# Optimization experiments

Hardware: AMD Instinct MI355X
Metric: run time of the kernel (lower is better)

Reference implementation:

```python
import jax, jax.numpy as jnp
import numpy as np

B, NP, NS = 64, 32, 72
H, F = 4, 64
HD = H * F            # 256
CS, CE = 7, 16
L = 4
NC = 110
EPS = 1e-6


def setup_inputs() -> dict:
    key = jax.random.key(0)
    ks = jax.random.split(key, 32)
    def n(k, shape, s=0.05):
        return (jax.random.normal(k, shape, jnp.float32) * s)
    spatial_obs = jax.random.normal(ks[0], (B, NP, NS), jnp.float32)
    card_context = jax.random.normal(ks[1], (B, CS, CE), jnp.float32)
    adj = (jax.random.uniform(ks[2], (NS, NS)) > 0.85).astype(jnp.float32)
    adj = jnp.maximum(adj, jnp.eye(NS, dtype=jnp.float32))  # self-loops
    return {
        'spatial_obs': spatial_obs,
        'card_context': card_context,
        'adj': adj,
        'ctx_W': n(ks[3], (CS * CE, HD)), 'ctx_b': jnp.zeros((HD,)),
        'lnc_s': jnp.ones((HD,)), 'lnc_b': jnp.zeros((HD,)),
        'in_W': n(ks[4], (NP, HD)), 'in_b': jnp.zeros((HD,)),
        'lnp_s': jnp.ones((L, HD)), 'lnp_b': jnp.zeros((L, HD)),
        'cp_W': n(ks[5], (L, HD, HD)), 'cp_b': jnp.zeros((L, HD)),
        'Wl': n(ks[6], (L, HD, HD)), 'Wr': n(ks[7], (L, HD, HD)),
        'Wa': n(ks[8], (L, H, F)),
        'op_W': n(ks[9], (L, HD, HD)), 'op_b': jnp.zeros((L, HD)),
        'card_W': n(ks[10], (HD, NC)), 'card_b': jnp.zeros((NC,)),
        'at_W': n(ks[11], (HD, 3)), 'at_b': jnp.zeros((3,)),
        'src_W': n(ks[12], (HD, NS)), 'src_b': jnp.zeros((NS,)),
        'tgt_W': n(ks[13], (HD, NS)), 'tgt_b': jnp.zeros((NS,)),
        'v1_W': n(ks[14], (HD, 128)), 'v1_b': jnp.zeros((128,)),
        'v2_W': n(ks[15], (128, 1)), 'v2_b': jnp.zeros((1,)),
    }


def _layernorm(x, s, b):
    m = jnp.mean(x, axis=-1, keepdims=True)
    v = jnp.var(x, axis=-1, keepdims=True)
    return (x - m) * jax.lax.rsqrt(v + EPS) * s + b


def _gatv2(h, adj, Wl, Wr, Wa):
    # h: (B, N, HD); GATv2: e_ij = Wa . LeakyReLU(Wl h_i + Wr h_j)
    b, n, _ = h.shape
    hl = jnp.einsum('bnd,de->bne', h, Wl).reshape(b, n, H, F)
    hr = jnp.einsum('bnd,de->bne', h, Wr).reshape(b, n, H, F)
    e = jax.nn.leaky_relu(hl[:, :, None, :, :] + hr[:, None, :, :, :], 0.2)  # (B,N,N,H,F)
    scores = jnp.einsum('bijhf,hf->bijh', e, Wa)
    scores = jnp.where(adj[None, :, :, None] > 0, scores, -1e9)
    attn = jax.nn.softmax(scores, axis=2)  # softmax over neighbors j
    out = jnp.einsum('bijh,bjhf->bihf', attn, hr)
    return out.reshape(b, n, HD)


def reference(spatial_obs, card_context, adj,
              ctx_W, ctx_b, lnc_s, lnc_b, in_W, in_b,
              lnp_s, lnp_b, cp_W, cp_b, Wl, Wr, Wa, op_W, op_b,
              card_W, card_b, at_W, at_b, src_W, src_b, tgt_W, tgt_b,
              v1_W, v1_b, v2_W, v2_b):
    b = spatial_obs.shape[0]
    ctx = card_context.reshape(b, CS * CE)
    g = jax.nn.relu(_layernorm(ctx @ ctx_W + ctx_b, lnc_s, lnc_b))  # (B, HD)
    x = jnp.einsum('bps,pd->bsd', spatial_obs, in_W) + in_b          # (B, NS, HD)
    for l in range(L):
        h = _layernorm(x, lnp_s[l], lnp_b[l])
        h = h + (g @ cp_W[l] + cp_b[l])[:, None, :]
        hg = _gatv2(h, adj, Wl[l], Wr[l], Wa[l])
        x = x + (hg @ op_W[l] + op_b[l])
    ge = jnp.mean(x, axis=1)  # (B, HD)
    card_logits = ge @ card_W + card_b
    action_type_logits = ge @ at_W + at_b
    src_logits = ge @ src_W + src_b
    tgt_logits = ge @ tgt_W + tgt_b
    value = jnp.tanh(jax.nn.relu(ge @ v1_W + v1_b) @ v2_W + v2_b)
    return (card_logits, action_type_logits, src_logits, tgt_logits, value)
```

## Files before the change

### kernel.cpp

```cpp
#include <hip/hip_runtime.h>
#include <hip/hip_bf16.h>
#include <math.h>

#define B 64
#define NP 32
#define NS 72
#define NH 4
#define NF 64
#define HD 256
#define CTXD 112
#define NL 4
#define NC 110
#define LN_EPS 1e-6f
#define GROWS 8

#define SH 68
#define SA 76

typedef __hip_bfloat16 bf16;

__device__ __forceinline__ float ldv(const float* p, int i) { return p[i]; }
__device__ __forceinline__ float ldv(const bf16* p, int i) { return __bfloat162float(p[i]); }
__device__ __forceinline__ void stv(float* p, int i, float v) { p[i] = v; }
__device__ __forceinline__ void stv(bf16* p, int i, float v) { p[i] = __float2bfloat16(v); }

__global__ void k_detect(const void* adj, int* flag) {
  if (threadIdx.x == 0 && blockIdx.x == 0) {
    *flag = (((const unsigned short*)adj)[0] == 0x3F80u) ? 1 : 0;
  }
}

__device__ __forceinline__ void block_reduce_2(float& a, float& b, float* sred, int t) {
  #pragma unroll
  for (int o = 32; o > 0; o >>= 1) { a += __shfl_down(a, o); b += __shfl_down(b, o); }
  if ((t & 63) == 0) { sred[(t >> 6) * 2] = a; sred[(t >> 6) * 2 + 1] = b; }
  __syncthreads();
  a = sred[0] + sred[2] + sred[4] + sred[6];
  b = sred[1] + sred[3] + sred[5] + sred[7];
}

template <typename T>
__device__ void ctx_body(const T* cardctx, const T* ctxW, const T* ctxb,
                         const T* lncs, const T* lncb, float* g,
                         float* sred, float* sctx) {
  int b = blockIdx.x, t = threadIdx.x;
  if (t < CTXD) sctx[t] = ldv(cardctx, b * CTXD + t);
  __syncthreads();
  float acc = ldv(ctxb, t);
  for (int k = 0; k < CTXD; ++k) acc += sctx[k] * ldv(ctxW, k * HD + t);
  float a = acc, bb = acc * acc;
  block_reduce_2(a, bb, sred, t);
  float mean = a * (1.f / HD);
  float var = bb * (1.f / HD) - mean * mean;
  float r = rsqrtf(var + LN_EPS);
  float v = (acc - mean) * r * ldv(lncs, t) + ldv(lncb, t);
  g[b * HD + t] = fmaxf(v, 0.f);
}
__global__ void __launch_bounds__(256) k_ctx(const void* cardctx, const void* ctxW, const void* ctxb,
                      const void* lncs, const void* lncb, float* g, const int* flag) {
  __shared__ float sred[8];
  __shared__ float sctx[CTXD];
  if (*flag) ctx_body<bf16>((const bf16*)cardctx, (const bf16*)ctxW, (const bf16*)ctxb,
                            (const bf16*)lncs, (const bf16*)lncb, g, sred, sctx);
  else ctx_body<float>((const float*)cardctx, (const float*)ctxW, (const float*)ctxb,
                       (const float*)lncs, (const float*)lncb, g, sred, sctx);
}

template <typename T>
__device__ void inproj_body(const T* spat, const T* inW, const T* inb, float* x, float* ssp) {
  int blk = blockIdx.x; int b = blk / NS; int s = blk % NS; int t = threadIdx.x;
  if (t < NP) ssp[t] = ldv(spat, (b * NP + t) * NS + s);
  __syncthreads();
  float acc = ldv(inb, t);
  #pragma unroll 8
  for (int p = 0; p < NP; ++p) acc += ssp[p] * ldv(inW, p * HD + t);
  x[blk * HD + t] = acc;
}
__global__ void __launch_bounds__(256) k_inproj(const void* spat, const void* inW, const void* inb,
                         float* x, const int* flag) {
  __shared__ float ssp[NP];
  if (*flag) inproj_body<bf16>((const bf16*)spat, (const bf16*)inW, (const bf16*)inb, x, ssp);
  else inproj_body<float>((const float*)spat, (const float*)inW, (const float*)inb, x, ssp);
}

template <typename T>
__device__ void cproj_body(const float* g, const T* cpW, const T* cpb, float* c, int l, float* sg) {
  int b = blockIdx.x, t = threadIdx.x;
  sg[t] = g[b * HD + t];
  __syncthreads();
  const T* W = cpW + l * HD * HD;
  float acc = ldv(cpb, l * HD + t);
  for (int k = 0; k < HD; ++k) acc += sg[k] * ldv(W, k * HD + t);
  c[b * HD + t] = acc;
}
__global__ void __launch_bounds__(256) k_cproj(const float* g, const void* cpW, const void* cpb,
                        float* c, int l, const int* flag) {
  __shared__ float sg[HD];
  if (*flag) cproj_body<bf16>(g, (const bf16*)cpW, (const bf16*)cpb, c, l, sg);
  else cproj_body<float>(g, (const float*)cpW, (const float*)cpb, c, l, sg);
}

template <typename T>
__device__ void lnadd_body(const float* x, const float* c, const T* lnps, const T* lnpb,
                           float* h, int l, float* sred) {
  int row = blockIdx.x, t = threadIdx.x;
  float v = x[row * HD + t];
  float a = v, bb = v * v;
  block_reduce_2(a, bb, sred, t);
  float mean = a * (1.f / HD);
  float var = bb * (1.f / HD) - mean * mean;
  float r = rsqrtf(var + LN_EPS);
  float o = (v - mean) * r * ldv(lnps, l * HD + t) + ldv(lnpb, l * HD + t)
          + c[(row / NS) * HD + t];
  h[row * HD + t] = o;
}
__global__ void __launch_bounds__(256) k_lnadd(const float* x, const float* c, const void* lnps, const void* lnpb,
                        float* h, int l, const int* flag) {
  __shared__ float sred[8];
  if (*flag) lnadd_body<bf16>(x, c, (const bf16*)lnps, (const bf16*)lnpb, h, l, sred);
  else lnadd_body<float>(x, c, (const float*)lnps, (const float*)lnpb, h, l, sred);
}

template <typename T>
__device__ void gemmlr_body(const float* h, const T* Wl, const T* Wr, float* hl, float* hr,
                            int l, float (*xs)[HD]) {
  int row0 = blockIdx.x * GROWS; int t = threadIdx.x;
  #pragma unroll
  for (int r = 0; r < GROWS; ++r) xs[r][t] = h[(row0 + r) * HD + t];
  __syncthreads();
  const T* Wlp = Wl + l * HD * HD;
  const T* Wrp = Wr + l * HD * HD;
  float acc[GROWS];
  #pragma unroll
  for (int r = 0; r < GROWS; ++r) acc[r] = 0.f;
  for (int k = 0; k < HD; ++k) {
    float w = ldv(Wlp, k * HD + t);
    #pragma unroll
    for (int r = 0; r < GROWS; ++r) acc[r] += xs[r][k] * w;
  }
  #pragma unroll
  for (int r = 0; r < GROWS; ++r) hl[(row0 + r) * HD + t] = acc[r];
  #pragma unroll
  for (int r = 0; r < GROWS; ++r) acc[r] = 0.f;
  for (int k = 0; k < HD; ++k) {
    float w = ldv(Wrp, k * HD + t);
    #pragma unroll
    for (int r = 0; r < GROWS; ++r) acc[r] += xs[r][k] * w;
  }
  #pragma unroll
  for (int r = 0; r < GROWS; ++r) hr[(row0 + r) * HD + t] = acc[r];
}
__global__ void __launch_bounds__(256) k_gemm_lr(const float* h, const void* Wl, const void* Wr,
                          float* hl, float* hr, int l, const int* flag) {
  __shared__ float xs[GROWS][HD];
  if (*flag) gemmlr_body<bf16>(h, (const bf16*)Wl, (const bf16*)Wr, hl, hr, l, xs);
  else gemmlr_body<float>(h, (const float*)Wl, (const float*)Wr, hl, hr, l, xs);
}

template <typename T>
__device__ void gat_body(const float* __restrict__ hl, const float* __restrict__ hr,
                         const T* __restrict__ adj, const T* __restrict__ Wa,
                         float* __restrict__ hg, int l,
                         float* hl_s, float* hr_s, float* attnT, float* wa04_s) {
  const int bid = blockIdx.x;
  const int b = bid >> 2, hh = bid & 3;
  const int t = threadIdx.x;
  const int w = t >> 6, L = t & 63;

  const float* hlbase = hl + (size_t)(b * NS) * HD + hh * NF;
  const float* hrbase = hr + (size_t)(b * NS) * HD + hh * NF;

  const float4* hrg1 = (const float4*)(hrbase + L * HD);
  const float4* hrg2 = (const float4*)(hrbase + (64 + (L & 7)) * HD);
  float4 hr1[16], hr2[16];
  #pragma unroll
  for (int q = 0; q < 16; ++q) hr1[q] = hrg1[q];
  #pragma unroll
  for (int q = 0; q < 16; ++q) hr2[q] = hrg2[q];

  if (t < NF) wa04_s[t] = 0.4f * ldv(Wa, l * HD + hh * NF + t);

  const float4* hlg4 = (const float4*)hlbase;
  const float4* hrg4 = (const float4*)hrbase;
  for (int c = t; c < NS * 16; c += 256) {
    int j = c >> 4, q = c & 15;
    *(float4*)&hl_s[j * SH + 4 * q] = hlg4[j * 64 + q];
    *(float4*)&hr_s[j * SH + 4 * q] = hrg4[j * 64 + q];
  }
  __syncthreads();

  float B1 = 0.f, B2 = 0.f;
  #pragma unroll
  for (int q = 0; q < 16; ++q) {
    float4 w4 = *(const float4*)&wa04_s[4 * q];
    B1 = fmaf(w4.x, hr1[q].x, B1); B1 = fmaf(w4.y, hr1[q].y, B1);
    B1 = fmaf(w4.z, hr1[q].z, B1); B1 = fmaf(w4.w, hr1[q].w, B1);
    B2 = fmaf(w4.x, hr2[q].x, B2); B2 = fmaf(w4.y, hr2[q].y, B2);
    B2 = fmaf(w4.z, hr2[q].z, B2); B2 = fmaf(w4.w, hr2[q].w, B2);
  }
  float B15_1 = 1.5f * B1, B15_2 = 1.5f * B2;
  float wa04L = wa04_s[L];

  for (int p = 0; p < 18; ++p) {
    int i = w + 4 * p;
    float av = wa04L * hl_s[i * SH + L];
    #pragma unroll
    for (int o = 32; o > 0; o >>= 1) av += __shfl_xor(av, o);
    float A15 = 1.5f * av;

    float acc1 = 0.f, acc2 = 0.f;
    #pragma unroll
    for (int q = 0; q < 16; ++q) {
      float4 h4 = *(const float4*)&hl_s[i * SH + 4 * q];
      float4 w4 = *(const float4*)&wa04_s[4 * q];
      float e;
      e = h4.x + hr1[q].x; acc1 = fmaf(w4.x, fabsf(e), acc1);
      e = h4.y + hr1[q].y; acc1 = fmaf(w4.y, fabsf(e), acc1);
      e = h4.z + hr1[q].z; acc1 = fmaf(w4.z, fabsf(e), acc1);
      e = h4.w + hr1[q].w; acc1 = fmaf(w4.w, fabsf(e), acc1);
      e = h4.x + hr2[q].x; acc2 = fmaf(w4.x, fabsf(e), acc2);
      e = h4.y + hr2[q].y; acc2 = fmaf(w4.y, fabsf(e), acc2);
      e = h4.z + hr2[q].z; acc2 = fmaf(w4.z, fabsf(e), acc2);
      e = h4.w + hr2[q].w; acc2 = fmaf(w4.w, fabsf(e), acc2);
    }
    float s1 = A15 + B15_1 + acc1;
    float s2 = A15 + B15_2 + acc2;
    float a1 = ldv(adj, i * NS + L);
    s1 = (a1 > 0.f) ? s1 : -1e30f;
    if (L < 8) {
      float a2 = ldv(adj, i * NS + 64 + L);
      s2 = (a2 > 0.f) ? s2 : -1e30f;
    } else {
      s2 = -1e30f;
    }
    float m = fmaxf(s1, s2);
    #pragma unroll
    for (int o = 32; o > 0; o >>= 1) m = fmaxf(m, __shfl_xor(m, o));
    float e1 = __expf(s1 - m);
    float e2 = __expf(s2 - m);
    float se = e1 + e2;
    #pragma unroll
    for (int o = 32; o > 0; o >>= 1) se += __shfl_xor(se, o);
    float inv = 1.f / se;
    attnT[L * SA + i] = e1 * inv;
    if (L < 8) attnT[(64 + L) * SA + i] = e2 * inv;
  }
  __syncthreads();

  for (int p = 0; p < 5; ++p) {
    int g = w + 4 * p;
    if (g >= 18) break;
    int i0 = 4 * g;
    float a0 = 0.f, a1 = 0.f, a2 = 0.f, a3 = 0.f;
    #pragma unroll 4
    for (int j = 0; j < NS; ++j) {
      float4 at = *(const float4*)&attnT[j * SA + i0];
      float hv = hr_s[j * SH + L];
      a0 = fmaf(at.x, hv, a0); a1 = fmaf(at.y, hv, a1);
      a2 = fmaf(at.z, hv, a2); a3 = fmaf(at.w, hv, a3);
    }
    float* o = hg + (size_t)(b * NS + i0) * HD + hh * NF + L;
    o[0] = a0; o[HD] = a1; o[2 * HD] = a2; o[3 * HD] = a3;
  }
}
__global__ void __launch_bounds__(256, 1) k_gat(const float* hl, const float* hr, const void* adj, const void* Wa,
                      float* hg, int l, const int* flag) {
  __shared__ float hl_s[NS * SH];
  __shared__ float hr_s[NS * SH];
  __shared__ float attnT[NS * SA];
  __shared__ float wa04_s[NF];
  if (*flag) gat_body<bf16>(hl, hr, (const bf16*)adj, (const bf16*)Wa, hg, l, hl_s, hr_s, attnT, wa04_s);
  else gat_body<float>(hl, hr, (const float*)adj, (const float*)Wa, hg, l, hl_s, hr_s, attnT, wa04_s);
}

template <typename T>
__device__ void gemmop_body(const float* hg, const T* opW, const T* opb, float* x,
                            int l, float (*xs)[HD]) {
  int row0 = blockIdx.x * GROWS; int t = threadIdx.x;
  #pragma unroll
  for (int r = 0; r < GROWS; ++r) xs[r][t] = hg[(row0 + r) * HD + t];
  __syncthreads();
  const T* W = opW + l * HD * HD;
  float acc[GROWS];
  #pragma unroll
  for (int r = 0; r < GROWS; ++r) acc[r] = 0.f;
  for (int k = 0; k < HD; ++k) {
    float w = ldv(W, k * HD + t);
    #pragma unroll
    for (int r = 0; r < GROWS; ++r) acc[r] += xs[r][k] * w;
  }
  float bias = ldv(opb, l * HD + t);
  #pragma unroll
  for (int r = 0; r < GROWS; ++r) x[(row0 + r) * HD + t] += acc[r] + bias;
}
__global__ void __launch_bounds__(256) k_gemm_op(const float* hg, const void* opW, const void* opb,
                          float* x, int l, const int* flag) {
  __shared__ float xs[GROWS][HD];
  if (*flag) gemmop_body<bf16>(hg, (const bf16*)opW, (const bf16*)opb, x, l, xs);
  else gemmop_body<float>(hg, (const float*)opW, (const float*)opb, x, l, xs);
}

template <typename T>
__device__ void heads_body(const float* x,
                           const T* cardW, const T* cardb, const T* atW, const T* atb,
                           const T* srcW, const T* srcb, const T* tgtW, const T* tgtb,
                           const T* v1W, const T* v1b, const T* v2W, const T* v2b,
                           T* out, float* sge, float* sh1) {
  int b = blockIdx.x, t = threadIdx.x;
  float acc = 0.f;
  for (int s = 0; s < NS; ++s) acc += x[(b * NS + s) * HD + t];
  sge[t] = acc * (1.f / NS);
  __syncthreads();
  for (int p = t; p < NC + 3 + NS + NS; p += 256) {
    if (p < NC) {
      int col = p;
      float o = ldv(cardb, col);
      for (int k = 0; k < HD; ++k) o += sge[k] * ldv(cardW, k * NC + col);
      stv(out, b * NC + col, o);
    } else if (p < NC + 3) {
      int col = p - NC;
      float o = ldv(atb, col);
      for (int k = 0; k < HD; ++k) o += sge[k] * ldv(atW, k * 3 + col);
      stv(out, B * NC + b * 3 + col, o);
    } else if (p < NC + 3 + NS) {
      int col = p - NC - 3;
      float o = ldv(srcb, col);
      for (int k = 0; k < HD; ++k) o += sge[k] * ldv(srcW, k * NS + col);
      stv(out, B * NC + B * 3 + b * NS + col, o);
    } else {
      int col = p - NC - 3 - NS;
      float o = ldv(tgtb, col);
      for (int k = 0; k < HD; ++k) o += sge[k] * ldv(tgtW, k * NS + col);
      stv(out, B * NC + B * 3 + B * NS + b * NS + col, o);
    }
  }
  if (t < 128) {
    float o = ldv(v1b, t);
    for (int k = 0; k < HD; ++k) o += sge[k] * ldv(v1W, k * 128 + t);
    sh1[t] = fmaxf(o, 0.f);
  }
  __syncthreads();
  if (t < 64) {
    float pv = sh1[t] * ldv(v2W, t) + sh1[t + 64] * ldv(v2W, t + 64);
    #pragma unroll
    for (int o = 32; o > 0; o >>= 1) pv += __shfl_xor(pv, o);
    if (t == 0) stv(out, B * (NC + 3 + NS + NS) + b, tanhf(pv + ldv(v2b, 0)));
  }
}
__global__ void __launch_bounds__(256) k_heads(const float* x,
                        const void* cardW, const void* cardb, const void* atW, const void* atb,
                        const void* srcW, const void* srcb, const void* tgtW, const void* tgtb,
                        const void* v1W, const void* v1b, const void* v2W, const void* v2b,
                        void* out, const int* flag) {
  __shared__ float sge[HD];
  __shared__ float sh1[128];
  if (*flag) heads_body<bf16>(x, (const bf16*)cardW, (const bf16*)cardb, (const bf16*)atW,
                              (const bf16*)atb, (const bf16*)srcW, (const bf16*)srcb,
                              (const bf16*)tgtW, (const bf16*)tgtb, (const bf16*)v1W,
                              (const bf16*)v1b, (const bf16*)v2W, (const bf16*)v2b,
                              (bf16*)out, sge, sh1);
  else heads_body<float>(x, (const float*)cardW, (const float*)cardb, (const float*)atW,
                         (const float*)atb, (const float*)srcW, (const float*)srcb,
                         (const float*)tgtW, (const float*)tgtb, (const float*)v1W,
                         (const float*)v1b, (const float*)v2W, (const float*)v2b,
                         (float*)out, sge, sh1);
}

extern "C" void kernel_launch(void* const* d_in, const int* in_sizes, int n_in,
                              void* d_out, int out_size, void* d_ws, size_t ws_size,
                              hipStream_t stream) {
  const void* spatial = d_in[0];
  const void* cardctx = d_in[1];
  const void* adj = d_in[2];
  const void* ctxW = d_in[3]; const void* ctxb = d_in[4];
  const void* lncs = d_in[5]; const void* lncb = d_in[6];
  const void* inW = d_in[7];  const void* inb = d_in[8];
  const void* lnps = d_in[9]; const void* lnpb = d_in[10];
  const void* cpW = d_in[11]; const void* cpb = d_in[12];
  const void* Wl = d_in[13];  const void* Wr = d_in[14]; const void* Wa = d_in[15];
  const void* opW = d_in[16]; const void* opb = d_in[17];
  const void* cardW = d_in[18]; const void* cardb = d_in[19];
  const void* atW = d_in[20];   const void* atb = d_in[21];
  const void* srcW = d_in[22];  const void* srcb = d_in[23];
  const void* tgtW = d_in[24];  const void* tgtb = d_in[25];
  const void* v1W = d_in[26];   const void* v1b = d_in[27];
  const void* v2W = d_in[28];   const void* v2b = d_in[29];

  int* flag = (int*)d_ws;
  float* base = (float*)((char*)d_ws + 256);
  float* g  = base;
  float* c  = g + B * HD;
  float* x  = c + B * HD;
  float* h  = x + B * NS * HD;
  float* hl = h + B * NS * HD;
  float* hr = hl + B * NS * HD;
  float* hg = h;

  k_detect<<<1, 64, 0, stream>>>(adj, flag);
  k_ctx<<<B, HD, 0, stream>>>(cardctx, ctxW, ctxb, lncs, lncb, g, flag);
  k_inproj<<<B * NS, HD, 0, stream>>>(spatial, inW, inb, x, flag);
  for (int l = 0; l < NL; ++l) {
    k_cproj<<<B, HD, 0, stream>>>(g, cpW, cpb, c, l, flag);
    k_lnadd<<<B * NS, HD, 0, stream>>>(x, c, lnps, lnpb, h, l, flag);
    k_gemm_lr<<<B * NS / GROWS, HD, 0, stream>>>(h, Wl, Wr, hl, hr, l, flag);
    k_gat<<<B * NH, 256, 0, stream>>>(hl, hr, adj, Wa, hg, l, flag);
    k_gemm_op<<<B * NS / GROWS, HD, 0, stream>>>(hg, opW, opb, x, l, flag);
  }
  k_heads<<<B, HD, 0, stream>>>(x, cardW, cardb, atW, atb, srcW, srcb, tgtW, tgtb,
                                v1W, v1b, v2W, v2b, d_out, flag);
}
```

Baseline: 652.7 us.

## Use bf16 MFMA for layer GEMMs with pre-transposed weights, split small projections

Adds a pre-pass that transposes and converts Wl, Wr and op_W to bf16 so the per-layer projection GEMMs can run on MFMA 16x16x32 bf16 instructions over 16-row tiles. LayerNorm and GAT kernels now also write bf16 copies of their outputs to feed these GEMMs. The context projection and the output heads are split across more blocks with K-partitioned partial sums to raise parallelism. The heads are split into mean, head GEMM and value kernels. This trades extra launches and bf16 write traffic for fewer scalar FMA loops; the fp32 path keeps a scalar fallback.

```diff
diff --git a/kernel.cpp b/kernel.cpp
--- a/kernel.cpp
+++ b/kernel.cpp
@@ -12,21 +12,50 @@
 #define NL 4
 #define NC 110
 #define LN_EPS 1e-6f
-#define GROWS 8
 
 #define SH 68
 #define SA 76
+#define ALD 264
 
 typedef __hip_bfloat16 bf16;
+typedef unsigned short u16;
+typedef __attribute__((ext_vector_type(8))) short short8;
+typedef __attribute__((ext_vector_type(4))) float floatx4;
 
 __device__ __forceinline__ float ldv(const float* p, int i) { return p[i]; }
 __device__ __forceinline__ float ldv(const bf16* p, int i) { return __bfloat162float(p[i]); }
 __device__ __forceinline__ void stv(float* p, int i, float v) { p[i] = v; }
 __device__ __forceinline__ void stv(bf16* p, int i, float v) { p[i] = __float2bfloat16(v); }
+__device__ __forceinline__ u16 f2bfbits(float v) {
+  bf16 h = __float2bfloat16(v);
+  return *(u16*)&h;
+}
 
 __global__ void k_detect(const void* adj, int* flag) {
   if (threadIdx.x == 0 && blockIdx.x == 0) {
-    *flag = (((const unsigned short*)adj)[0] == 0x3F80u) ? 1 : 0;
+    *flag = (((const u16*)adj)[0] == 0x3F80u) ? 1 : 0;
+  }
+}
+
+__global__ void __launch_bounds__(256) k_wt(const void* Wl, const void* Wr, const void* opW,
+                                            u16* WT, const int* flag) {
+  __shared__ u16 tl[64 * 65];
+  int mat = blockIdx.x >> 4, tile = blockIdx.x & 15;
+  int k0 = (tile >> 2) * 64, n0 = (tile & 3) * 64;
+  const void* src = (mat < 4) ? Wl : (mat < 8) ? Wr : opW;
+  int lmat = mat & 3;
+  int t = threadIdx.x;
+  bool isb = (*flag != 0);
+  for (int i = 0; i < 16; ++i) {
+    int idx = i * 256 + t; int k = idx >> 6, n = idx & 63;
+    size_t off = (size_t)lmat * 65536 + (size_t)(k0 + k) * 256 + n0 + n;
+    float v = isb ? __bfloat162float(((const bf16*)src)[off]) : ((const float*)src)[off];
+    tl[n * 65 + k] = f2bfbits(v);
+  }
+  __syncthreads();
+  for (int i = 0; i < 16; ++i) {
+    int idx = i * 256 + t; int n = idx >> 6, k = idx & 63;
+    WT[(size_t)mat * 65536 + (size_t)(n0 + n) * 256 + k0 + k] = tl[n * 65 + k];
   }
 }
 
@@ -84,25 +113,36 @@
 }
 
 template <typename T>
-__device__ void cproj_body(const float* g, const T* cpW, const T* cpb, float* c, int l, float* sg) {
-  int b = blockIdx.x, t = threadIdx.x;
+__device__ void cproj2_body(const float* g, const T* cpW, const T* cpb, float* c, int l,
+                            float* sg, float (*part)[64]) {
+  int b = blockIdx.x >> 2, ch = blockIdx.x & 3;
+  int t = threadIdx.x;
   sg[t] = g[b * HD + t];
   __syncthreads();
-  const T* W = cpW + l * HD * HD;
-  float acc = ldv(cpb, l * HD + t);
-  for (int k = 0; k < HD; ++k) acc += sg[k] * ldv(W, k * HD + t);
-  c[b * HD + t] = acc;
-}
-__global__ void __launch_bounds__(256) k_cproj(const float* g, const void* cpW, const void* cpb,
+  int col = ch * 64 + (t & 63), s = t >> 6, kb = s * 64;
+  const T* W = cpW + (size_t)l * HD * HD;
+  float p = 0.f;
+  #pragma unroll 8
+  for (int k = 0; k < 64; ++k) p += sg[kb + k] * ldv(W, (kb + k) * HD + col);
+  part[s][t & 63] = p;
+  __syncthreads();
+  if (t < 64) {
+    int col2 = ch * 64 + t;
+    c[b * HD + col2] = part[0][t] + part[1][t] + part[2][t] + part[3][t]
+                     + ldv(cpb, l * HD + col2);
+  }
+}
+__global__ void __launch_bounds__(256) k_cproj2(const float* g, const void* cpW, const void* cpb,
                         float* c, int l, const int* flag) {
   __shared__ float sg[HD];
-  if (*flag) cproj_body<bf16>(g, (const bf16*)cpW, (const bf16*)cpb, c, l, sg);
-  else cproj_body<float>(g, (const float*)cpW, (const float*)cpb, c, l, sg);
+  __shared__ float part[4][64];
+  if (*flag) cproj2_body<bf16>(g, (const bf16*)cpW, (const bf16*)cpb, c, l, sg, part);
+  else cproj2_body<float>(g, (const float*)cpW, (const float*)cpb, c, l, sg, part);
 }
 
 template <typename T>
 __device__ void lnadd_body(const float* x, const float* c, const T* lnps, const T* lnpb,
-                           float* h, int l, float* sred) {
+                           float* h, bf16* hb, int l, float* sred) {
   int row = blockIdx.x, t = threadIdx.x;
   float v = x[row * HD + t];
   float a = v, bb = v * v;
@@ -113,54 +153,117 @@
   float o = (v - mean) * r * ldv(lnps, l * HD + t) + ldv(lnpb, l * HD + t)
           + c[(row / NS) * HD + t];
   h[row * HD + t] = o;
+  hb[row * HD + t] = __float2bfloat16(o);
 }
 __global__ void __launch_bounds__(256) k_lnadd(const float* x, const float* c, const void* lnps, const void* lnpb,
-                        float* h, int l, const int* flag) {
+                        float* h, bf16* hb, int l, const int* flag) {
   __shared__ float sred[8];
-  if (*flag) lnadd_body<bf16>(x, c, (const bf16*)lnps, (const bf16*)lnpb, h, l, sred);
-  else lnadd_body<float>(x, c, (const float*)lnps, (const float*)lnpb, h, l, sred);
-}
-
-template <typename T>
-__device__ void gemmlr_body(const float* h, const T* Wl, const T* Wr, float* hl, float* hr,
-                            int l, float (*xs)[HD]) {
-  int row0 = blockIdx.x * GROWS; int t = threadIdx.x;
-  #pragma unroll
-  for (int r = 0; r < GROWS; ++r) xs[r][t] = h[(row0 + r) * HD + t];
-  __syncthreads();
-  const T* Wlp = Wl + l * HD * HD;
-  const T* Wrp = Wr + l * HD * HD;
-  float acc[GROWS];
-  #pragma unroll
-  for (int r = 0; r < GROWS; ++r) acc[r] = 0.f;
+  if (*flag) lnadd_body<bf16>(x, c, (const bf16*)lnps, (const bf16*)lnpb, h, hb, l, sred);
+  else lnadd_body<float>(x, c, (const float*)lnps, (const float*)lnpb, h, hb, l, sred);
+}
+
+template <bool ACC>
+__device__ void mfma16(const bf16* __restrict__ Ab, const u16* __restrict__ WT,
+                       float* __restrict__ out, int M0,
+                       const bf16* __restrict__ bias, int boff, u16* A_s) {
+  int t = threadIdx.x;
+  {
+    int row = t >> 4, off = (t & 15) * 16;
+    const u16* src = (const u16*)Ab + (M0 + row) * HD + off;
+    *(short8*)&A_s[row * ALD + off] = *(const short8*)src;
+    *(short8*)&A_s[row * ALD + off + 8] = *(const short8*)(src + 8);
+  }
+  __syncthreads();
+  int w = t >> 6, L = t & 63;
+  int n0 = w * 64;
+  int q = L >> 4, m16 = L & 15;
+  floatx4 acc0 = {0.f, 0.f, 0.f, 0.f};
+  floatx4 acc1 = acc0, acc2 = acc0, acc3 = acc0;
+  const u16* ap = A_s + m16 * ALD + q * 8;
+  const u16* bp = WT + (size_t)(n0 + m16) * HD + q * 8;
+  #pragma unroll
+  for (int ks = 0; ks < 8; ++ks) {
+    short8 a = *(const short8*)(ap + ks * 32);
+    short8 b0 = *(const short8*)(bp + ks * 32);
+    short8 b1 = *(const short8*)(bp + 16 * HD + ks * 32);
+    short8 b2 = *(const short8*)(bp + 32 * HD + ks * 32);
+    short8 b3 = *(const short8*)(bp + 48 * HD + ks * 32);
+    acc0 = __builtin_amdgcn_mfma_f32_16x16x32_bf16(a, b0, acc0, 0, 0, 0);
+    acc1 = __builtin_amdgcn_mfma_f32_16x16x32_bf16(a, b1, acc1, 0, 0, 0);
+    acc2 = __builtin_amdgcn_mfma_f32_16x16x32_bf16(a, b2, acc2, 0, 0, 0);
+    acc3 = __builtin_amdgcn_mfma_f32_16x16x32_bf16(a, b3, acc3, 0, 0, 0);
+  }
+  #pragma unroll
+  for (int nt = 0; nt < 4; ++nt) {
+    floatx4 a4 = (nt == 0) ? acc0 : (nt == 1) ? acc1 : (nt == 2) ? acc2 : acc3;
+    int col = n0 + nt * 16 + m16;
+    float bv = ACC ? __bfloat162float(bias[boff + col]) : 0.f;
+    #pragma unroll
+    for (int r = 0; r < 4; ++r) {
+      int idx = (M0 + q * 4 + r) * HD + col;
+      float v = a4[r] + bv;
+      if (ACC) v += out[idx];
+      out[idx] = v;
+    }
+  }
+}
+
+__device__ void vec16(const float* A, const float* W, float* out, int M0, bool accf,
+                      const float* bias, int boff, float* xs) {
+  int t = threadIdx.x;
+  for (int i = 0; i < 16; ++i) xs[i * HD + t] = A[(M0 + i) * HD + t];
+  __syncthreads();
+  float acc[16];
+  #pragma unroll
+  for (int r = 0; r < 16; ++r) acc[r] = 0.f;
   for (int k = 0; k < HD; ++k) {
-    float w = ldv(Wlp, k * HD + t);
+    float wv = W[k * HD + t];
     #pragma unroll
-    for (int r = 0; r < GROWS; ++r) acc[r] += xs[r][k] * w;
-  }
-  #pragma unroll
-  for (int r = 0; r < GROWS; ++r) hl[(row0 + r) * HD + t] = acc[r];
-  #pragma unroll
-  for (int r = 0; r < GROWS; ++r) acc[r] = 0.f;
-  for (int k = 0; k < HD; ++k) {
-    float w = ldv(Wrp, k * HD + t);
-    #pragma unroll
-    for (int r = 0; r < GROWS; ++r) acc[r] += xs[r][k] * w;
-  }
-  #pragma unroll
-  for (int r = 0; r < GROWS; ++r) hr[(row0 + r) * HD + t] = acc[r];
-}
-__global__ void __launch_bounds__(256) k_gemm_lr(const float* h, const void* Wl, const void* Wr,
-                          float* hl, float* hr, int l, const int* flag) {
-  __shared__ float xs[GROWS][HD];
-  if (*flag) gemmlr_body<bf16>(h, (const bf16*)Wl, (const bf16*)Wr, hl, hr, l, xs);
-  else gemmlr_body<float>(h, (const float*)Wl, (const float*)Wr, hl, hr, l, xs);
+    for (int r = 0; r < 16; ++r) acc[r] += xs[r * HD + k] * wv;
+  }
+  for (int r = 0; r < 16; ++r) {
+    float v = acc[r];
+    if (accf) v += out[(M0 + r) * HD + t] + bias[boff + t];
+    out[(M0 + r) * HD + t] = v;
+  }
+}
+
+__global__ void __launch_bounds__(256) k_gemm_lr2(const bf16* hb, const float* hf, const u16* WT,
+                         const void* Wl, const void* Wr,
+                         float* hl, float* hr, int l, const int* flag) {
+  __shared__ u16 A_s[16 * ALD];
+  __shared__ float xs[16 * HD];
+  bool second = blockIdx.x >= 288;
+  int M0 = (second ? blockIdx.x - 288 : blockIdx.x) * 16;
+  float* out = second ? hr : hl;
+  if (*flag) {
+    const u16* wt = WT + (size_t)((second ? 4 : 0) + l) * 65536;
+    mfma16<false>(hb, wt, out, M0, nullptr, 0, A_s);
+  } else {
+    const float* W = (const float*)(second ? Wr : Wl) + (size_t)l * 65536;
+    vec16(hf, W, out, M0, false, nullptr, 0, xs);
+  }
+}
+
+__global__ void __launch_bounds__(256) k_gemm_op2(const bf16* hgb, const float* hgf, const u16* WT,
+                         const void* opW, const void* opb,
+                         float* x, int l, const int* flag) {
+  __shared__ u16 A_s[16 * ALD];
+  __shared__ float xs[16 * HD];
+  int M0 = blockIdx.x * 16;
+  if (*flag) {
+    const u16* wt = WT + (size_t)(8 + l) * 65536;
+    mfma16<true>(hgb, wt, x, M0, (const bf16*)opb, l * HD, A_s);
+  } else {
+    const float* W = (const float*)opW + (size_t)l * 65536;
+    vec16(hgf, W, x, M0, true, (const float*)opb, l * HD, xs);
+  }
 }
 
 template <typename T>
 __device__ void gat_body(const float* __restrict__ hl, const float* __restrict__ hr,
                          const T* __restrict__ adj, const T* __restrict__ Wa,
-                         float* __restrict__ hg, int l,
+                         float* __restrict__ hg, bf16* __restrict__ hgb, int l,
                          float* hl_s, float* hr_s, float* attnT, float* wa04_s) {
   const int bid = blockIdx.x;
   const int b = bid >> 2, hh = bid & 3;
@@ -259,111 +362,93 @@
       a0 = fmaf(at.x, hv, a0); a1 = fmaf(at.y, hv, a1);
       a2 = fmaf(at.z, hv, a2); a3 = fmaf(at.w, hv, a3);
     }
-    float* o = hg + (size_t)(b * NS + i0) * HD + hh * NF + L;
-    o[0] = a0; o[HD] = a1; o[2 * HD] = a2; o[3 * HD] = a3;
+    size_t o = (size_t)(b * NS + i0) * HD + hh * NF + L;
+    hg[o] = a0; hg[o + HD] = a1; hg[o + 2 * HD] = a2; hg[o + 3 * HD] = a3;
+    hgb[o] = __float2bfloat16(a0); hgb[o + HD] = __float2bfloat16(a1);
+    hgb[o + 2 * HD] = __float2bfloat16(a2); hgb[o + 3 * HD] = __float2bfloat16(a3);
   }
 }
 __global__ void __launch_bounds__(256, 1) k_gat(const float* hl, const float* hr, const void* adj, const void* Wa,
-                      float* hg, int l, const int* flag) {
+                      float* hg, bf16* hgb, int l, const int* flag) {
   __shared__ float hl_s[NS * SH];
   __shared__ float hr_s[NS * SH];
   __shared__ float attnT[NS * SA];
   __shared__ float wa04_s[NF];
-  if (*flag) gat_body<bf16>(hl, hr, (const bf16*)adj, (const bf16*)Wa, hg, l, hl_s, hr_s, attnT, wa04_s);
-  else gat_body<float>(hl, hr, (const float*)adj, (const float*)Wa, hg, l, hl_s, hr_s, attnT, wa04_s);
-}
-
-template <typename T>
-__device__ void gemmop_body(const float* hg, const T* opW, const T* opb, float* x,
-                            int l, float (*xs)[HD]) {
-  int row0 = blockIdx.x * GROWS; int t = threadIdx.x;
-  #pragma unroll
-  for (int r = 0; r < GROWS; ++r) xs[r][t] = hg[(row0 + r) * HD + t];
-  __syncthreads();
-  const T* W = opW + l * HD * HD;
-  float acc[GROWS];
-  #pragma unroll
-  for (int r = 0; r < GROWS; ++r) acc[r] = 0.f;
-  for (int k = 0; k < HD; ++k) {
-    float w = ldv(W, k * HD + t);
-    #pragma unroll
-    for (int r = 0; r < GROWS; ++r) acc[r] += xs[r][k] * w;
-  }
-  float bias = ldv(opb, l * HD + t);
-  #pragma unroll
-  for (int r = 0; r < GROWS; ++r) x[(row0 + r) * HD + t] += acc[r] + bias;
-}
-__global__ void __launch_bounds__(256) k_gemm_op(const float* hg, const void* opW, const void* opb,
-                          float* x, int l, const int* flag) {
-  __shared__ float xs[GROWS][HD];
-  if (*flag) gemmop_body<bf16>(hg, (const bf16*)opW, (const bf16*)opb, x, l, xs);
-  else gemmop_body<float>(hg, (const float*)opW, (const float*)opb, x, l, xs);
-}
-
-template <typename T>
-__device__ void heads_body(const float* x,
-                           const T* cardW, const T* cardb, const T* atW, const T* atb,
-                           const T* srcW, const T* srcb, const T* tgtW, const T* tgtb,
-                           const T* v1W, const T* v1b, const T* v2W, const T* v2b,
-                           T* out, float* sge, float* sh1) {
+  if (*flag) gat_body<bf16>(hl, hr, (const bf16*)adj, (const bf16*)Wa, hg, hgb, l, hl_s, hr_s, attnT, wa04_s);
+  else gat_body<float>(hl, hr, (const float*)adj, (const float*)Wa, hg, hgb, l, hl_s, hr_s, attnT, wa04_s);
+}
+
+__global__ void __launch_bounds__(256) k_ge(const float* x, float* ge) {
   int b = blockIdx.x, t = threadIdx.x;
-  float acc = 0.f;
-  for (int s = 0; s < NS; ++s) acc += x[(b * NS + s) * HD + t];
-  sge[t] = acc * (1.f / NS);
-  __syncthreads();
-  for (int p = t; p < NC + 3 + NS + NS; p += 256) {
-    if (p < NC) {
-      int col = p;
-      float o = ldv(cardb, col);
-      for (int k = 0; k < HD; ++k) o += sge[k] * ldv(cardW, k * NC + col);
-      stv(out, b * NC + col, o);
-    } else if (p < NC + 3) {
-      int col = p - NC;
-      float o = ldv(atb, col);
-      for (int k = 0; k < HD; ++k) o += sge[k] * ldv(atW, k * 3 + col);
-      stv(out, B * NC + b * 3 + col, o);
-    } else if (p < NC + 3 + NS) {
-      int col = p - NC - 3;
-      float o = ldv(srcb, col);
-      for (int k = 0; k < HD; ++k) o += sge[k] * ldv(srcW, k * NS + col);
-      stv(out, B * NC + B * 3 + b * NS + col, o);
-    } else {
-      int col = p - NC - 3 - NS;
-      float o = ldv(tgtb, col);
-      for (int k = 0; k < HD; ++k) o += sge[k] * ldv(tgtW, k * NS + col);
-      stv(out, B * NC + B * 3 + B * NS + b * NS + col, o);
-    }
-  }
-  if (t < 128) {
-    float o = ldv(v1b, t);
-    for (int k = 0; k < HD; ++k) o += sge[k] * ldv(v1W, k * 128 + t);
-    sh1[t] = fmaxf(o, 0.f);
-  }
+  float a = 0.f;
+  for (int s = 0; s < NS; ++s) a += x[(b * NS + s) * HD + t];
+  ge[b * HD + t] = a * (1.f / NS);
+}
+
+template <typename T>
+__device__ void heads2_body(const float* ge,
+                            const T* cardW, const T* cardb, const T* atW, const T* atb,
+                            const T* srcW, const T* srcb, const T* tgtW, const T* tgtb,
+                            const T* v1W, const T* v1b, T* out, float* r1,
+                            float* sge, float (*part)[64]) {
+  int b = blockIdx.x / 7, ch = blockIdx.x % 7;
+  int t = threadIdx.x;
+  sge[t] = ge[b * HD + t];
+  __syncthreads();
+  int c = ch * 64 + (t & 63);
+  int s = t >> 6;
+  const T* W = nullptr; int ld = 0, cc = 0;
+  if (c < 110)      { W = cardW; ld = 110; cc = c; }
+  else if (c < 113) { W = atW;   ld = 3;   cc = c - 110; }
+  else if (c < 185) { W = srcW;  ld = 72;  cc = c - 113; }
+  else if (c < 257) { W = tgtW;  ld = 72;  cc = c - 185; }
+  else if (c < 385) { W = v1W;   ld = 128; cc = c - 257; }
+  float p = 0.f;
+  if (W) {
+    int kb = s * 64;
+    #pragma unroll 8
+    for (int k = 0; k < 64; ++k) p += sge[kb + k] * ldv(W, (kb + k) * ld + cc);
+  }
+  part[s][t & 63] = p;
   __syncthreads();
   if (t < 64) {
-    float pv = sh1[t] * ldv(v2W, t) + sh1[t + 64] * ldv(v2W, t + 64);
-    #pragma unroll
-    for (int o = 32; o > 0; o >>= 1) pv += __shfl_xor(pv, o);
-    if (t == 0) stv(out, B * (NC + 3 + NS + NS) + b, tanhf(pv + ldv(v2b, 0)));
-  }
-}
-__global__ void __launch_bounds__(256) k_heads(const float* x,
+    int c2 = ch * 64 + t;
+    float v = part[0][t] + part[1][t] + part[2][t] + part[3][t];
+    if (c2 < 110)      stv(out, b * 110 + c2, v + ldv(cardb, c2));
+    else if (c2 < 113) stv(out, 7040 + b * 3 + (c2 - 110), v + ldv(atb, c2 - 110));
+    else if (c2 < 185) stv(out, 7232 + b * 72 + (c2 - 113), v + ldv(srcb, c2 - 113));
+    else if (c2 < 257) stv(out, 11840 + b * 72 + (c2 - 185), v + ldv(tgtb, c2 - 185));
+    else if (c2 < 385) r1[b * 128 + (c2 - 257)] = fmaxf(v + ldv(v1b, c2 - 257), 0.f);
+  }
+}
+__global__ void __launch_bounds__(256) k_heads2(const float* ge,
                         const void* cardW, const void* cardb, const void* atW, const void* atb,
                         const void* srcW, const void* srcb, const void* tgtW, const void* tgtb,
-                        const void* v1W, const void* v1b, const void* v2W, const void* v2b,
-                        void* out, const int* flag) {
+                        const void* v1W, const void* v1b, void* out, float* r1, const int* flag) {
   __shared__ float sge[HD];
-  __shared__ float sh1[128];
-  if (*flag) heads_body<bf16>(x, (const bf16*)cardW, (const bf16*)cardb, (const bf16*)atW,
-                              (const bf16*)atb, (const bf16*)srcW, (const bf16*)srcb,
-                              (const bf16*)tgtW, (const bf16*)tgtb, (const bf16*)v1W,
-                              (const bf16*)v1b, (const bf16*)v2W, (const bf16*)v2b,
-                              (bf16*)out, sge, sh1);
-  else heads_body<float>(x, (const float*)cardW, (const float*)cardb, (const float*)atW,
-                         (const float*)atb, (const float*)srcW, (const float*)srcb,
-                         (const float*)tgtW, (const float*)tgtb, (const float*)v1W,
-                         (const float*)v1b, (const float*)v2W, (const float*)v2b,
-                         (float*)out, sge, sh1);
+  __shared__ float part[4][64];
+  if (*flag) heads2_body<bf16>(ge, (const bf16*)cardW, (const bf16*)cardb, (const bf16*)atW,
+                               (const bf16*)atb, (const bf16*)srcW, (const bf16*)srcb,
+                               (const bf16*)tgtW, (const bf16*)tgtb, (const bf16*)v1W,
+                               (const bf16*)v1b, (bf16*)out, r1, sge, part);
+  else heads2_body<float>(ge, (const float*)cardW, (const float*)cardb, (const float*)atW,
+                          (const float*)atb, (const float*)srcW, (const float*)srcb,
+                          (const float*)tgtW, (const float*)tgtb, (const float*)v1W,
+                          (const float*)v1b, (float*)out, r1, sge, part);
+}
+
+template <typename T>
+__device__ void value_body(const float* r1, const T* v2W, const T* v2b, T* out) {
+  int b = blockIdx.x, t = threadIdx.x;
+  float v = r1[b * 128 + t] * ldv(v2W, t) + r1[b * 128 + 64 + t] * ldv(v2W, 64 + t);
+  #pragma unroll
+  for (int o = 32; o > 0; o >>= 1) v += __shfl_xor(v, o);
+  if (t == 0) stv(out, 16448 + b, tanhf(v + ldv(v2b, 0)));
+}
+__global__ void __launch_bounds__(64) k_value(const float* r1, const void* v2W, const void* v2b,
+                       void* out, const int* flag) {
+  if (*flag) value_body<bf16>(r1, (const bf16*)v2W, (const bf16*)v2b, (bf16*)out);
+  else value_body<float>(r1, (const float*)v2W, (const float*)v2b, (float*)out);
 }
 
 extern "C" void kernel_launch(void* const* d_in, const int* in_sizes, int n_in,
@@ -388,24 +473,32 @@
 
   int* flag = (int*)d_ws;
   float* base = (float*)((char*)d_ws + 256);
-  float* g  = base;
-  float* c  = g + B * HD;
-  float* x  = c + B * HD;
-  float* h  = x + B * NS * HD;
-  float* hl = h + B * NS * HD;
-  float* hr = hl + B * NS * HD;
-  float* hg = h;
+  float* g   = base;
+  float* c   = g + B * HD;
+  float* x   = c + B * HD;
+  float* hf  = x + B * NS * HD;
+  float* hl  = hf + B * NS * HD;
+  float* hr  = hl + B * NS * HD;
+  float* ge  = hr + B * NS * HD;
+  float* r1  = ge + B * HD;
+  u16* breg  = (u16*)(r1 + B * 128);
+  bf16* hb   = (bf16*)breg;
+  bf16* hgb  = hb + B * NS * HD;
+  u16* WT    = (u16*)(hgb + B * NS * HD);
 
   k_detect<<<1, 64, 0, stream>>>(adj, flag);
+  k_wt<<<192, 256, 0, stream>>>(Wl, Wr, opW, WT, flag);
   k_ctx<<<B, HD, 0, stream>>>(cardctx, ctxW, ctxb, lncs, lncb, g, flag);
   k_inproj<<<B * NS, HD, 0, stream>>>(spatial, inW, inb, x, flag);
   for (int l = 0; l < NL; ++l) {
-    k_cproj<<<B, HD, 0, stream>>>(g, cpW, cpb, c, l, flag);
-    k_lnadd<<<B * NS, HD, 0, stream>>>(x, c, lnps, lnpb, h, l, flag);
-    k_gemm_lr<<<B * NS / GROWS, HD, 0, stream>>>(h, Wl, Wr, hl, hr, l, flag);
-    k_gat<<<B * NH, 256, 0, stream>>>(hl, hr, adj, Wa, hg, l, flag);
-    k_gemm_op<<<B * NS / GROWS, HD, 0, stream>>>(hg, opW, opb, x, l, flag);
-  }
-  k_heads<<<B, HD, 0, stream>>>(x, cardW, cardb, atW, atb, srcW, srcb, tgtW, tgtb,
-                                v1W, v1b, v2W, v2b, d_out, flag);
-}
+    k_cproj2<<<B * 4, HD, 0, stream>>>(g, cpW, cpb, c, l, flag);
+    k_lnadd<<<B * NS, HD, 0, stream>>>(x, c, lnps, lnpb, hf, hb, l, flag);
+    k_gemm_lr2<<<576, 256, 0, stream>>>(hb, hf, WT, Wl, Wr, hl, hr, l, flag);
+    k_gat<<<B * NH, 256, 0, stream>>>(hl, hr, adj, Wa, hf, hgb, l, flag);
+    k_gemm_op2<<<288, 256, 0, stream>>>(hgb, hf, WT, opW, opb, x, l, flag);
+  }
+  k_ge<<<B, HD, 0, stream>>>(x, ge);
+  k_heads2<<<B * 7, 256, 0, stream>>>(ge, cardW, cardb, atW, atb, srcW, srcb, tgtW, tgtb,
+                                      v1W, v1b, d_out, r1, flag);
+  k_value<<<B, 64, 0, stream>>>(r1, v2W, v2b, d_out, flag);
+}
```

Result: slower. 973.6 us (+49.2%).
